# Kernel optimization log

Measured on AMD Instinct MI355X. Metric: run time of the kernel, lower is better.

The kernel has to match this reference:

```python
import jax, jax.numpy as jnp
import numpy as np

EMBED_DIM = 1024
N_HEADS = 16
HEAD_DIM = EMBED_DIM // N_HEADS
SCALE = 1.0 / np.sqrt(HEAD_DIM)


def setup_inputs() -> dict:
    key = jax.random.key(0)
    ks = jax.random.split(key, 11)
    B, S, D = 4, 2048, EMBED_DIM
    lim = 1.0 / np.sqrt(D)
    def lin(kk):
        kw, kb = jax.random.split(kk)
        W = jax.random.uniform(kw, (D, D), jnp.float32, -lim, lim)
        b = jax.random.uniform(kb, (D,), jnp.float32, -lim, lim)
        return W, b
    Wq, bq = lin(ks[0])
    Wk, bk = lin(ks[1])
    Wv, bv = lin(ks[2])
    Wo, bo = lin(ks[3])
    q = jax.random.normal(ks[4], (B, S, D), jnp.float32)
    k = jax.random.normal(ks[5], (B, S, D), jnp.float32)
    v = jax.random.normal(ks[6], (B, S, D), jnp.float32)
    return {"q": q, "k": k, "v": v,
            "Wq": Wq, "bq": bq, "Wk": Wk, "bk": bk,
            "Wv": Wv, "bv": bv, "Wo": Wo, "bo": bo}


def reference(q, k, v, Wq, bq, Wk, bk, Wv, bv, Wo, bo):
    B, Sq, D = q.shape
    Sk = k.shape[1]
    # linear projections (torch Linear: x @ W.T + b)
    qh = (q @ Wq.T + bq).reshape(B, Sq, N_HEADS, HEAD_DIM).transpose(0, 2, 1, 3)
    kh = (k @ Wk.T + bk).reshape(B, Sk, N_HEADS, HEAD_DIM).transpose(0, 2, 1, 3)
    vh = (v @ Wv.T + bv).reshape(B, Sk, N_HEADS, HEAD_DIM).transpose(0, 2, 1, 3)
    # scaled dot-product attention, no mask, dropout_p=0
    scores = jnp.einsum('bhqd,bhkd->bhqk', qh, kh) * SCALE  # [B,H,Sq,Sk]
    weights = jax.nn.softmax(scores, axis=-1)
    ctx = jnp.einsum('bhqk,bhkd->bhqd', weights, vh)
    ctx = ctx.transpose(0, 2, 1, 3).reshape(B, Sq, D)
    return ctx @ Wo.T + bo
```

## Files before the change

### kernel.cpp

```cpp
#include <hip/hip_runtime.h>
#include <hip/hip_bf16.h>
#include <stdint.h>

#define B_SZ 4
#define SEQ  2048
#define DM   1024
#define NH   16
#define HD   64
#define MTOT (B_SZ*SEQ)
#define QS_LOG2E 0.18033688011112042f
#define M0SHIFT  24.0f

typedef __attribute__((ext_vector_type(8))) short bf16x8;
typedef __attribute__((ext_vector_type(4))) float f32x4;

#if __has_builtin(__builtin_amdgcn_exp2f)
__device__ __forceinline__ float fexp2(float x) { return __builtin_amdgcn_exp2f(x); }
#else
__device__ __forceinline__ float fexp2(float x) {
  float r; asm("v_exp_f32 %0, %1" : "=v"(r) : "v"(x)); return r;
}
#endif

__device__ __forceinline__ unsigned short f2b(float f) {
  union { float f; unsigned int i; } v; v.f = f;
  unsigned int r = v.i + 0x7fffu + ((v.i >> 16) & 1u);
  return (unsigned short)(r >> 16);
}

#define GPTR __attribute__((address_space(1)))
#define LPTR __attribute__((address_space(3)))
__device__ __forceinline__ void gl_lds16(const void* g, void* l) {
  __builtin_amdgcn_global_load_lds((GPTR const unsigned int*)g,
                                   (LPTR unsigned int*)l, 16, 0, 0);
}

__global__ __launch_bounds__(256) void conv3(const float* __restrict__ a,
                                             const float* __restrict__ b,
                                             const float* __restrict__ c,
                                             unsigned short* __restrict__ oa,
                                             unsigned short* __restrict__ ob,
                                             unsigned short* __restrict__ oc,
                                             int n) {
  const float* in = (blockIdx.z == 0) ? a : (blockIdx.z == 1) ? b : c;
  unsigned short* out = (blockIdx.z == 0) ? oa : (blockIdx.z == 1) ? ob : oc;
  int i = (blockIdx.x * 256 + threadIdx.x) * 8;
  int stride = gridDim.x * 256 * 8;
  for (; i < n; i += stride) {
    float4 x = *(const float4*)(in + i);
    float4 y = *(const float4*)(in + i + 4);
    ushort4 u0; u0.x = f2b(x.x); u0.y = f2b(x.y); u0.z = f2b(x.z); u0.w = f2b(x.w);
    ushort4 u1; u1.x = f2b(y.x); u1.y = f2b(y.y); u1.z = f2b(y.z); u1.w = f2b(y.w);
    *(ushort4*)(out + i)     = u0;
    *(ushort4*)(out + i + 4) = u1;
  }
}
__global__ __launch_bounds__(256) void conv4(const float* __restrict__ a,
                                             const float* __restrict__ b,
                                             const float* __restrict__ c,
                                             const float* __restrict__ d,
                                             unsigned short* __restrict__ oa,
                                             unsigned short* __restrict__ ob,
                                             unsigned short* __restrict__ oc,
                                             unsigned short* __restrict__ od,
                                             int n) {
  const float* in = (blockIdx.z == 0) ? a : (blockIdx.z == 1) ? b
                  : (blockIdx.z == 2) ? c : d;
  unsigned short* out = (blockIdx.z == 0) ? oa : (blockIdx.z == 1) ? ob
                      : (blockIdx.z == 2) ? oc : od;
  int i = (blockIdx.x * 256 + threadIdx.x) * 8;
  int stride = gridDim.x * 256 * 8;
  for (; i < n; i += stride) {
    float4 x = *(const float4*)(in + i);
    float4 y = *(const float4*)(in + i + 4);
    ushort4 u0; u0.x = f2b(x.x); u0.y = f2b(x.y); u0.z = f2b(x.z); u0.w = f2b(x.w);
    ushort4 u1; u1.x = f2b(y.x); u1.y = f2b(y.y); u1.z = f2b(y.z); u1.w = f2b(y.w);
    *(ushort4*)(out + i)     = u0;
    *(ushort4*)(out + i + 4) = u1;
  }
}

__device__ __forceinline__ void stage_glds(const unsigned short* __restrict__ src,
                                           int ld, char* lds, int t) {
  const int gbase = t & ~63;
  const int lane  = t & 63;
  #pragma unroll
  for (int i = 0; i < 4; ++i) {
    int gb  = i*256 + gbase;
    int g   = gb + lane;
    int row = g >> 3;
    int cg  = (g & 7) ^ (row & 7);
    gl_lds16(src + (size_t)row*ld + cg*8, lds + (size_t)gb*16);
  }
}
__device__ __forceinline__ void stage_f32(const float* __restrict__ src, int ld,
                                          unsigned short* lds, int t) {
  #pragma unroll
  for (int i = 0; i < 8; ++i) {
    int e   = i*1024 + t*4;
    int row = e >> 6;
    int c4  = (e >> 2) & 15;
    float4 f = *(const float4*)(src + (size_t)row*ld + c4*4);
    ushort4 u;
    u.x = f2b(f.x); u.y = f2b(f.y); u.z = f2b(f.z); u.w = f2b(f.w);
    int hi = (row*64 + c4*4) ^ ((row & 7) << 3);
    *(ushort4*)&lds[hi] = u;
  }
}

template<int AF32, int BF32, int OUTF32>
__global__ __launch_bounds__(256, 2) void gemm_bias(
    const void* __restrict__ Xv,
    const void* __restrict__ Wv,
    const float* __restrict__ bias,
    void* __restrict__ Cout,
    int M, int N, int Kd, float oscale)
{
  __shared__ __align__(16) unsigned short As[128*64];
  __shared__ __align__(16) unsigned short Bs[128*64];
  const int t    = threadIdx.x;
  const int lane = t & 63;
  const int w    = t >> 6;
  const int wm   = w >> 1, wn = w & 1;
  const int m0   = blockIdx.y * 128;
  const int n0   = blockIdx.x * 128;

  f32x4 acc[4][4] = {};

  for (int k0 = 0; k0 < Kd; k0 += 64) {
    __syncthreads();
    if (AF32) stage_f32((const float*)Xv + (size_t)m0*Kd + k0, Kd, As, t);
    else      stage_glds((const unsigned short*)Xv + (size_t)m0*Kd + k0, Kd, (char*)As, t);
    if (BF32) stage_f32((const float*)Wv + (size_t)n0*Kd + k0, Kd, Bs, t);
    else      stage_glds((const unsigned short*)Wv + (size_t)n0*Kd + k0, Kd, (char*)Bs, t);
    __syncthreads();

    #pragma unroll
    for (int kk = 0; kk < 2; ++kk) {
      bf16x8 af[4], bfr[4];
      #pragma unroll
      for (int mt = 0; mt < 4; ++mt) {
        int r  = wm*64 + mt*16 + (lane & 15);
        int hi = (r*64 + kk*32 + (lane >> 4)*8) ^ ((r & 7) << 3);
        af[mt] = *(const bf16x8*)&As[hi];
      }
      #pragma unroll
      for (int nt = 0; nt < 4; ++nt) {
        int r  = wn*64 + nt*16 + (lane & 15);
        int hi = (r*64 + kk*32 + (lane >> 4)*8) ^ ((r & 7) << 3);
        bfr[nt] = *(const bf16x8*)&Bs[hi];
      }
      #pragma unroll
      for (int mt = 0; mt < 4; ++mt)
        #pragma unroll
        for (int nt = 0; nt < 4; ++nt)
          acc[mt][nt] = __builtin_amdgcn_mfma_f32_16x16x32_bf16(
              af[mt], bfr[nt], acc[mt][nt], 0, 0, 0);
    }
  }

  #pragma unroll
  for (int nt = 0; nt < 4; ++nt) {
    int col = n0 + wn*64 + nt*16 + (lane & 15);
    float bv = bias[col];
    #pragma unroll
    for (int mt = 0; mt < 4; ++mt) {
      #pragma unroll
      for (int j = 0; j < 4; ++j) {
        int rrow = m0 + wm*64 + mt*16 + (lane >> 4)*4 + j;
        float val = (acc[mt][nt][j] + bv) * oscale;
        if (OUTF32)
          ((float*)Cout)[(size_t)rrow*N + col] = val;
        else
          ((unsigned short*)Cout)[(size_t)rrow*N + col] = f2b(val);
      }
    }
  }
}

__global__ __launch_bounds__(256, 2) void attn_fwd(
    const unsigned short* __restrict__ Qb,
    const unsigned short* __restrict__ Kb,
    const unsigned short* __restrict__ Vb,
    unsigned short* __restrict__ Ob)
{
  __shared__ __align__(16) unsigned short Buf[4][64*64];

  const int t    = threadIdx.x;
  const int lane = t & 63;
  const int w    = t >> 6;
  const int l15  = lane & 15;
  const int quad = lane >> 4;
  const int bh   = blockIdx.y;
  const int b    = bh >> 4, h = bh & 15;
  const int q0   = blockIdx.x * 128;
  const int gbase = t & ~63;

  const size_t headoff = ((size_t)b*SEQ)*DM + (size_t)h*HD;
  const unsigned short* Qh = Qb + headoff;
  const unsigned short* Kh = Kb + headoff;
  const unsigned short* Vh = Vb + headoff;

  const int jp   = (t & 31) * 2;
  const int seg  = t >> 5;
  const int slot0 = ((jp >> 5) & 1)*32 + ((jp >> 2) & 3)*8 + ((jp >> 4) & 1)*4 + (jp & 3);
  const unsigned short* vsrc = Vh + (size_t)jp*DM + seg*8;

  {
    unsigned short* Qlds = &Buf[2][0];
    #pragma unroll
    for (int i = 0; i < 4; ++i) {
      int gb  = i*256 + gbase;
      int g   = gb + lane;
      int row = g >> 3;
      int cg  = (g & 7) ^ (row & 7);
      gl_lds16(Qh + (size_t)(q0 + row)*DM + cg*8, (char*)Qlds + (size_t)gb*16);
    }
  }
  bf16x8 pvA0 = *(const bf16x8*)(vsrc);
  bf16x8 pvA1 = *(const bf16x8*)(vsrc + DM);
  bf16x8 pvB0 = *(const bf16x8*)(vsrc + 64*DM);
  bf16x8 pvB1 = *(const bf16x8*)(vsrc + 65*DM);
  __syncthreads();

  bf16x8 qfA[2], qfB[2];
  {
    const unsigned short* Qlds = &Buf[2][0];
    #pragma unroll
    for (int kk = 0; kk < 2; ++kk) {
      int rA  = w*32 + l15;
      int rB  = w*32 + 16 + l15;
      qfA[kk] = *(const bf16x8*)&Qlds[(rA*64 + kk*32 + quad*8) ^ ((rA & 7) << 3)];
      qfB[kk] = *(const bf16x8*)&Qlds[(rB*64 + kk*32 + quad*8) ^ ((rB & 7) << 3)];
    }
  }
  auto writeV = [&](const bf16x8& v0, const bf16x8& v1, unsigned short* dst) {
    #pragma unroll
    for (int e = 0; e < 8; ++e) {
      int d = seg*8 + e;
      unsigned int pk = (unsigned int)(unsigned short)v0[e]
                      | ((unsigned int)(unsigned short)v1[e] << 16);
      *(unsigned int*)&dst[(d*64 + slot0) ^ ((d & 7) << 3)] = pk;
    }
  };
  writeV(pvA0, pvA1, Buf[0]);
  writeV(pvB0, pvB1, Buf[1]);
  __syncthreads();

  auto stageK = [&](int kv0, unsigned short* dst) {
    #pragma unroll
    for (int i = 0; i < 2; ++i) {
      int gb  = i*256 + gbase;
      int g   = gb + lane;
      int row = g >> 3;
      int cg  = (g & 7) ^ (row & 7);
      gl_lds16(Kh + (size_t)(kv0 + row)*DM + cg*8, (char*)dst + (size_t)gb*16);
    }
  };
  stageK(0,  Buf[2]);
  stageK(64, Buf[3]);
  __syncthreads();

  float lA = 0.f, lB = 0.f;
  f32x4 oA[4] = {}, oB[4] = {};
  const f32x4 mseed = {-M0SHIFT, -M0SHIFT, -M0SHIFT, -M0SHIFT};

  auto tile = [&](const unsigned short* Kc, const unsigned short* Vc) {
    f32x4 sA[4] = {mseed, mseed, mseed, mseed};
    f32x4 sB[4] = {mseed, mseed, mseed, mseed};
    __builtin_amdgcn_s_setprio(1);
    #pragma unroll
    for (int kk = 0; kk < 2; ++kk) {
      #pragma unroll
      for (int nt = 0; nt < 4; ++nt) {
        int r  = nt*16 + l15;
        int hi = (r*64 + kk*32 + quad*8) ^ ((r & 7) << 3);
        bf16x8 kf = *(const bf16x8*)&Kc[hi];
        sA[nt] = __builtin_amdgcn_mfma_f32_16x16x32_bf16(kf, qfA[kk], sA[nt], 0, 0, 0);
        sB[nt] = __builtin_amdgcn_mfma_f32_16x16x32_bf16(kf, qfB[kk], sB[nt], 0, 0, 0);
      }
    }
    __builtin_amdgcn_s_setprio(0);

    union { bf16x8 v; unsigned int u[4]; } PA0, PA1, PB0, PB1;
    {
      float p[4][4]; float rs = 0.f;
      #pragma unroll
      for (int nt = 0; nt < 4; ++nt)
        #pragma unroll
        for (int j = 0; j < 4; ++j) { p[nt][j] = fexp2(sA[nt][j]); rs += p[nt][j]; }
      lA += rs;
      #pragma unroll
      for (int k2 = 0; k2 < 4; ++k2) {
        int nt = k2 >> 1, a = (k2 & 1)*2;
        asm("v_cvt_pk_bf16_f32 %0, %1, %2" : "=v"(PA0.u[k2]) : "v"(p[nt][a]), "v"(p[nt][a+1]));
        asm("v_cvt_pk_bf16_f32 %0, %1, %2" : "=v"(PA1.u[k2]) : "v"(p[2+nt][a]), "v"(p[2+nt][a+1]));
      }
    }
    {
      float p[4][4]; float rs = 0.f;
      #pragma unroll
      for (int nt = 0; nt < 4; ++nt)
        #pragma unroll
        for (int j = 0; j < 4; ++j) { p[nt][j] = fexp2(sB[nt][j]); rs += p[nt][j]; }
      lB += rs;
      #pragma unroll
      for (int k2 = 0; k2 < 4; ++k2) {
        int nt = k2 >> 1, a = (k2 & 1)*2;
        asm("v_cvt_pk_bf16_f32 %0, %1, %2" : "=v"(PB0.u[k2]) : "v"(p[nt][a]), "v"(p[nt][a+1]));
        asm("v_cvt_pk_bf16_f32 %0, %1, %2" : "=v"(PB1.u[k2]) : "v"(p[2+nt][a]), "v"(p[2+nt][a+1]));
      }
    }

    __builtin_amdgcn_s_setprio(1);
    #pragma unroll
    for (int ks = 0; ks < 2; ++ks) {
      bf16x8 pfA = ks ? PA1.v : PA0.v;
      bf16x8 pfB = ks ? PB1.v : PB0.v;
      #pragma unroll
      for (int dt = 0; dt < 4; ++dt) {
        int d  = dt*16 + l15;
        int hi = (d*64 + ks*32 + quad*8) ^ ((d & 7) << 3);
        bf16x8 vf = *(const bf16x8*)&Vc[hi];
        oA[dt] = __builtin_amdgcn_mfma_f32_16x16x32_bf16(vf, pfA, oA[dt], 0, 0, 0);
        oB[dt] = __builtin_amdgcn_mfma_f32_16x16x32_bf16(vf, pfB, oB[dt], 0, 0, 0);
      }
    }
    __builtin_amdgcn_s_setprio(0);
  };

  for (int tk = 0; tk < SEQ/64; tk += 2) {
    const bool pa = (tk + 2 < SEQ/64);
    const bool pb = (tk + 3 < SEQ/64);
    if (pa) {
      const unsigned short* s = vsrc + (size_t)(tk + 2)*64*DM;
      pvA0 = *(const bf16x8*)(s);
      pvA1 = *(const bf16x8*)(s + DM);
    }
    tile(Buf[2], Buf[0]);
    __syncthreads();
    if (pa) { stageK((tk + 2)*64, Buf[2]); writeV(pvA0, pvA1, Buf[0]); }
    if (pb) {
      const unsigned short* s = vsrc + (size_t)(tk + 3)*64*DM;
      pvB0 = *(const bf16x8*)(s);
      pvB1 = *(const bf16x8*)(s + DM);
    }
    tile(Buf[3], Buf[1]);
    __syncthreads();
    if (pb) { stageK((tk + 3)*64, Buf[3]); writeV(pvB0, pvB1, Buf[1]); }
  }

  {
    float la = lA, lb = lB;
    la += __shfl_xor(la, 16); la += __shfl_xor(la, 32);
    lb += __shfl_xor(lb, 16); lb += __shfl_xor(lb, 32);
    float rla = 1.0f / la, rlb = 1.0f / lb;
    int qrowA = q0 + w*32 + l15;
    int qrowB = qrowA + 16;
    #pragma unroll
    for (int dt = 0; dt < 4; ++dt) {
      ushort4 u;
      u.x = f2b(oA[dt][0]*rla); u.y = f2b(oA[dt][1]*rla);
      u.z = f2b(oA[dt][2]*rla); u.w = f2b(oA[dt][3]*rla);
      *(ushort4*)&Ob[headoff + (size_t)qrowA*DM + dt*16 + quad*4] = u;
      ushort4 v;
      v.x = f2b(oB[dt][0]*rlb); v.y = f2b(oB[dt][1]*rlb);
      v.z = f2b(oB[dt][2]*rlb); v.w = f2b(oB[dt][3]*rlb);
      *(ushort4*)&Ob[headoff + (size_t)qrowB*DM + dt*16 + quad*4] = v;
    }
  }
}

extern "C" void kernel_launch(void* const* d_in, const int* in_sizes, int n_in,
                              void* d_out, int out_size, void* d_ws, size_t ws_size,
                              hipStream_t stream) {
  const float* q  = (const float*)d_in[0];
  const float* k  = (const float*)d_in[1];
  const float* v  = (const float*)d_in[2];
  const float* Wq = (const float*)d_in[3];
  const float* bq = (const float*)d_in[4];
  const float* Wk = (const float*)d_in[5];
  const float* bk = (const float*)d_in[6];
  const float* Wv = (const float*)d_in[7];
  const float* bv = (const float*)d_in[8];
  const float* Wo = (const float*)d_in[9];
  const float* bo = (const float*)d_in[10];

  const size_t MD  = (size_t)MTOT * DM;
  const size_t WSZ = (size_t)DM * DM;
  unsigned short* ws = (unsigned short*)d_ws;

  dim3 blk(256);
  dim3 gproj(DM/128, MTOT/128);
  dim3 gattn(SEQ/128, B_SZ*NH);

  const size_t need_big = (6*MD + 4*WSZ) * 2;
  const size_t need_mid = (4*MD + 1*WSZ) * 2;

  if (ws_size >= need_big) {
    unsigned short* qB  = ws;
    unsigned short* kB  = ws + MD;
    unsigned short* vB  = ws + 2*MD;
    unsigned short* Qp  = ws + 3*MD;
    unsigned short* Kp  = ws + 4*MD;
    unsigned short* Vp  = ws + 5*MD;
    unsigned short* WqB = ws + 6*MD;
    unsigned short* WkB = WqB + WSZ;
    unsigned short* WvB = WqB + 2*WSZ;
    unsigned short* WoB = WqB + 3*WSZ;
    unsigned short* Cp  = qB;

    hipLaunchKernelGGL(conv3, dim3(1024,1,3), blk, 0, stream, q, k, v, qB, kB, vB, (int)MD);
    hipLaunchKernelGGL(conv4, dim3(512,1,4),  blk, 0, stream, Wq, Wk, Wv, Wo, WqB, WkB, WvB, WoB, (int)WSZ);

    hipLaunchKernelGGL((gemm_bias<0,0,0>), gproj, blk, 0, stream, (const void*)qB, (const void*)WqB, bq, (void*)Qp, MTOT, DM, DM, QS_LOG2E);
    hipLaunchKernelGGL((gemm_bias<0,0,0>), gproj, blk, 0, stream, (const void*)kB, (const void*)WkB, bk, (void*)Kp, MTOT, DM, DM, 1.0f);
    hipLaunchKernelGGL((gemm_bias<0,0,0>), gproj, blk, 0, stream, (const void*)vB, (const void*)WvB, bv, (void*)Vp, MTOT, DM, DM, 1.0f);
    hipLaunchKernelGGL(attn_fwd, gattn, blk, 0, stream, Qp, Kp, Vp, Cp);
    hipLaunchKernelGGL((gemm_bias<0,0,1>), gproj, blk, 0, stream, (const void*)Cp, (const void*)WoB, bo, d_out, MTOT, DM, DM, 1.0f);
  } else if (ws_size >= need_mid) {
    unsigned short* Qp  = ws;
    unsigned short* Kp  = ws + MD;
    unsigned short* Vp  = ws + 2*MD;
    unsigned short* Cp  = ws + 3*MD;
    unsigned short* WqB = Cp;
    unsigned short* WkB = Cp + WSZ;
    unsigned short* WvB = Cp + 2*WSZ;
    unsigned short* WoB = ws + 4*MD;

    hipLaunchKernelGGL(conv4, dim3(512,1,4), blk, 0, stream, Wq, Wk, Wv, Wo, WqB, WkB, WvB, WoB, (int)WSZ);

    hipLaunchKernelGGL((gemm_bias<1,0,0>), gproj, blk, 0, stream, (const void*)q, (const void*)WqB, bq, (void*)Qp, MTOT, DM, DM, QS_LOG2E);
    hipLaunchKernelGGL((gemm_bias<1,0,0>), gproj, blk, 0, stream, (const void*)k, (const void*)WkB, bk, (void*)Kp, MTOT, DM, DM, 1.0f);
    hipLaunchKernelGGL((gemm_bias<1,0,0>), gproj, blk, 0, stream, (const void*)v, (const void*)WvB, bv, (void*)Vp, MTOT, DM, DM, 1.0f);
    hipLaunchKernelGGL(attn_fwd, gattn, blk, 0, stream, Qp, Kp, Vp, Cp);
    hipLaunchKernelGGL((gemm_bias<0,0,1>), gproj, blk, 0, stream, (const void*)Cp, (const void*)WoB, bo, d_out, MTOT, DM, DM, 1.0f);
  } else {
    unsigned short* Qp = ws;
    unsigned short* Kp = ws + MD;
    unsigned short* Vp = ws + 2*MD;
    unsigned short* Cp = ws + 3*MD;

    hipLaunchKernelGGL((gemm_bias<1,1,0>), gproj, blk, 0, stream, (const void*)q, (const void*)Wq, bq, (void*)Qp, MTOT, DM, DM, QS_LOG2E);
    hipLaunchKernelGGL((gemm_bias<1,1,0>), gproj, blk, 0, stream, (const void*)k, (const void*)Wk, bk, (void*)Kp, MTOT, DM, DM, 1.0f);
    hipLaunchKernelGGL((gemm_bias<1,1,0>), gproj, blk, 0, stream, (const void*)v, (const void*)Wv, bv, (void*)Vp, MTOT, DM, DM, 1.0f);
    hipLaunchKernelGGL(attn_fwd, gattn, blk, 0, stream, Qp, Kp, Vp, Cp);
    hipLaunchKernelGGL((gemm_bias<0,1,1>), gproj, blk, 0, stream, (const void*)Cp, (const void*)Wo, bo, d_out, MTOT, DM, DM, 1.0f);
  }
}
```

Before: 225.7 us.

## Batch QKV projections into one launch, merge conversions, remap attention blocks

Merges the activation and weight bf16 conversion kernels into a single seven-slice launch and fuses the three Q/K/V projection GEMMs into one grid with a z dimension, using a new dedicated bf16-only GEMM core. It also remaps the attention block index so that consecutive blocks are spread across heads and query tiles, likely to improve cache or XCD locality. The goal is to cut launch count and tail effects and to raise per-launch occupancy. The trade-off is a new GEMM core that may differ in performance from the templated one, for example if it lacks pipelining.

```diff
diff --git a/kernel.cpp b/kernel.cpp
--- a/kernel.cpp
+++ b/kernel.cpp
@@ -35,15 +35,8 @@
                                    (LPTR unsigned int*)l, 16, 0, 0);
 }
 
-__global__ __launch_bounds__(256) void conv3(const float* __restrict__ a,
-                                             const float* __restrict__ b,
-                                             const float* __restrict__ c,
-                                             unsigned short* __restrict__ oa,
-                                             unsigned short* __restrict__ ob,
-                                             unsigned short* __restrict__ oc,
-                                             int n) {
-  const float* in = (blockIdx.z == 0) ? a : (blockIdx.z == 1) ? b : c;
-  unsigned short* out = (blockIdx.z == 0) ? oa : (blockIdx.z == 1) ? ob : oc;
+__device__ __forceinline__ void conv_body(const float* __restrict__ in,
+                                          unsigned short* __restrict__ out, int n) {
   int i = (blockIdx.x * 256 + threadIdx.x) * 8;
   int stride = gridDim.x * 256 * 8;
   for (; i < n; i += stride) {
@@ -54,6 +47,21 @@
     *(ushort4*)(out + i)     = u0;
     *(ushort4*)(out + i + 4) = u1;
   }
+}
+__global__ __launch_bounds__(256) void conv7(
+    const float* __restrict__ q, const float* __restrict__ k, const float* __restrict__ v,
+    const float* __restrict__ Wq, const float* __restrict__ Wk,
+    const float* __restrict__ Wv, const float* __restrict__ Wo,
+    unsigned short* __restrict__ oq, unsigned short* __restrict__ ok,
+    unsigned short* __restrict__ ov, unsigned short* __restrict__ oWq,
+    unsigned short* __restrict__ oWk, unsigned short* __restrict__ oWv,
+    unsigned short* __restrict__ oWo, int nAct, int nW) {
+  const int z = blockIdx.z;
+  const float* in = (z == 0) ? q : (z == 1) ? k : (z == 2) ? v
+                  : (z == 3) ? Wq : (z == 4) ? Wk : (z == 5) ? Wv : Wo;
+  unsigned short* out = (z == 0) ? oq : (z == 1) ? ok : (z == 2) ? ov
+                      : (z == 3) ? oWq : (z == 4) ? oWk : (z == 5) ? oWv : oWo;
+  conv_body(in, out, (z < 3) ? nAct : nW);
 }
 __global__ __launch_bounds__(256) void conv4(const float* __restrict__ a,
                                              const float* __restrict__ b,
@@ -68,16 +76,7 @@
                   : (blockIdx.z == 2) ? c : d;
   unsigned short* out = (blockIdx.z == 0) ? oa : (blockIdx.z == 1) ? ob
                       : (blockIdx.z == 2) ? oc : od;
-  int i = (blockIdx.x * 256 + threadIdx.x) * 8;
-  int stride = gridDim.x * 256 * 8;
-  for (; i < n; i += stride) {
-    float4 x = *(const float4*)(in + i);
-    float4 y = *(const float4*)(in + i + 4);
-    ushort4 u0; u0.x = f2b(x.x); u0.y = f2b(x.y); u0.z = f2b(x.z); u0.w = f2b(x.w);
-    ushort4 u1; u1.x = f2b(y.x); u1.y = f2b(y.y); u1.z = f2b(y.z); u1.w = f2b(y.w);
-    *(ushort4*)(out + i)     = u0;
-    *(ushort4*)(out + i + 4) = u1;
-  }
+  conv_body(in, out, n);
 }
 
 __device__ __forceinline__ void stage_glds(const unsigned short* __restrict__ src,
@@ -106,6 +105,82 @@
     int hi = (row*64 + c4*4) ^ ((row & 7) << 3);
     *(ushort4*)&lds[hi] = u;
   }
+}
+
+__device__ __forceinline__ void gemm_core_bb(
+    const unsigned short* __restrict__ X, const unsigned short* __restrict__ W,
+    const float* __restrict__ bias, unsigned short* __restrict__ C,
+    float oscale, int m0, int n0, int t,
+    unsigned short* As, unsigned short* Bs)
+{
+  const int lane = t & 63;
+  const int w    = t >> 6;
+  const int wm   = w >> 1, wn = w & 1;
+
+  f32x4 acc[4][4] = {};
+
+  for (int k0 = 0; k0 < DM; k0 += 64) {
+    __syncthreads();
+    stage_glds(X + (size_t)m0*DM + k0, DM, (char*)As, t);
+    stage_glds(W + (size_t)n0*DM + k0, DM, (char*)Bs, t);
+    __syncthreads();
+
+    #pragma unroll
+    for (int kk = 0; kk < 2; ++kk) {
+      bf16x8 af[4], bfr[4];
+      #pragma unroll
+      for (int mt = 0; mt < 4; ++mt) {
+        int r  = wm*64 + mt*16 + (lane & 15);
+        int hi = (r*64 + kk*32 + (lane >> 4)*8) ^ ((r & 7) << 3);
+        af[mt] = *(const bf16x8*)&As[hi];
+      }
+      #pragma unroll
+      for (int nt = 0; nt < 4; ++nt) {
+        int r  = wn*64 + nt*16 + (lane & 15);
+        int hi = (r*64 + kk*32 + (lane >> 4)*8) ^ ((r & 7) << 3);
+        bfr[nt] = *(const bf16x8*)&Bs[hi];
+      }
+      #pragma unroll
+      for (int mt = 0; mt < 4; ++mt)
+        #pragma unroll
+        for (int nt = 0; nt < 4; ++nt)
+          acc[mt][nt] = __builtin_amdgcn_mfma_f32_16x16x32_bf16(
+              af[mt], bfr[nt], acc[mt][nt], 0, 0, 0);
+    }
+  }
+
+  #pragma unroll
+  for (int nt = 0; nt < 4; ++nt) {
+    int col = n0 + wn*64 + nt*16 + (lane & 15);
+    float bv = bias[col];
+    #pragma unroll
+    for (int mt = 0; mt < 4; ++mt) {
+      #pragma unroll
+      for (int j = 0; j < 4; ++j) {
+        int rrow = m0 + wm*64 + mt*16 + (lane >> 4)*4 + j;
+        C[(size_t)rrow*DM + col] = f2b((acc[mt][nt][j] + bv) * oscale);
+      }
+    }
+  }
+}
+
+__global__ __launch_bounds__(256, 2) void gemm_qkv(
+    const unsigned short* __restrict__ Xb, const unsigned short* __restrict__ Wb,
+    const float* __restrict__ b0, const float* __restrict__ b1,
+    const float* __restrict__ b2, unsigned short* __restrict__ Cb, float os0)
+{
+  __shared__ __align__(16) unsigned short As[128*64];
+  __shared__ __align__(16) unsigned short Bs[128*64];
+  const int z = blockIdx.z;
+  const size_t MD  = (size_t)MTOT * DM;
+  const size_t WSZ = (size_t)DM * DM;
+  const unsigned short* X = Xb + (size_t)z * MD;
+  const unsigned short* W = Wb + (size_t)z * WSZ;
+  const float* bias = (z == 0) ? b0 : (z == 1) ? b1 : b2;
+  unsigned short* C = Cb + (size_t)z * MD;
+  float oscale = (z == 0) ? os0 : 1.0f;
+  gemm_core_bb(X, W, bias, C, oscale,
+               blockIdx.y * 128, blockIdx.x * 128, threadIdx.x, As, Bs);
 }
 
 template<int AF32, int BF32, int OUTF32>
@@ -191,9 +266,14 @@
   const int w    = t >> 6;
   const int l15  = lane & 15;
   const int quad = lane >> 4;
-  const int bh   = blockIdx.y;
+
+  const int id   = blockIdx.x + (int)gridDim.x * blockIdx.y;
+  const int r_   = id & 7;
+  const int j_   = id >> 3;
+  const int bh   = r_*8 + (j_ >> 4);
+  const int qt   = j_ & 15;
   const int b    = bh >> 4, h = bh & 15;
-  const int q0   = blockIdx.x * 128;
+  const int q0   = qt * 128;
   const int gbase = t & ~63;
 
   const size_t headoff = ((size_t)b*SEQ)*DM + (size_t)h*HD;
@@ -405,17 +485,17 @@
     unsigned short* Kp  = ws + 4*MD;
     unsigned short* Vp  = ws + 5*MD;
     unsigned short* WqB = ws + 6*MD;
-    unsigned short* WkB = WqB + WSZ;
-    unsigned short* WvB = WqB + 2*WSZ;
     unsigned short* WoB = WqB + 3*WSZ;
     unsigned short* Cp  = qB;
 
-    hipLaunchKernelGGL(conv3, dim3(1024,1,3), blk, 0, stream, q, k, v, qB, kB, vB, (int)MD);
-    hipLaunchKernelGGL(conv4, dim3(512,1,4),  blk, 0, stream, Wq, Wk, Wv, Wo, WqB, WkB, WvB, WoB, (int)WSZ);
-
-    hipLaunchKernelGGL((gemm_bias<0,0,0>), gproj, blk, 0, stream, (const void*)qB, (const void*)WqB, bq, (void*)Qp, MTOT, DM, DM, QS_LOG2E);
-    hipLaunchKernelGGL((gemm_bias<0,0,0>), gproj, blk, 0, stream, (const void*)kB, (const void*)WkB, bk, (void*)Kp, MTOT, DM, DM, 1.0f);
-    hipLaunchKernelGGL((gemm_bias<0,0,0>), gproj, blk, 0, stream, (const void*)vB, (const void*)WvB, bv, (void*)Vp, MTOT, DM, DM, 1.0f);
+    hipLaunchKernelGGL(conv7, dim3(1024,1,7), blk, 0, stream,
+                       q, k, v, Wq, Wk, Wv, Wo,
+                       qB, kB, vB, WqB, WqB + WSZ, WqB + 2*WSZ, WoB,
+                       (int)MD, (int)WSZ);
+
+    hipLaunchKernelGGL(gemm_qkv, dim3(DM/128, MTOT/128, 3), blk, 0, stream,
+                       qB, WqB, bq, bk, bv, Qp, QS_LOG2E);
+
     hipLaunchKernelGGL(attn_fwd, gattn, blk, 0, stream, Qp, Kp, Vp, Cp);
     hipLaunchKernelGGL((gemm_bias<0,0,1>), gproj, blk, 0, stream, (const void*)Cp, (const void*)WoB, bo, d_out, MTOT, DM, DM, 1.0f);
   } else if (ws_size >= need_mid) {
```

Measured after the change: 216.8 us. 1.04x faster.
